# Performance work log

Measured on AMD Instinct MI355X. Metric: run time of the kernel, lower is better.

The kernel has to match this reference:

```python
import jax, jax.numpy as jnp
import numpy as np

COST_CLASS = 1.0
COST_REG = 1.0
NUM_TGT = 5  # targets per batch element, implied by `sizes = [5] * ...`

# All 5^5 = 3125 ways for each of the 5 targets to pick one of its 5 cheapest queries.
_CHOICES = np.stack(np.meshgrid(*([np.arange(NUM_TGT)] * NUM_TGT), indexing='ij'), -1).reshape(-1, NUM_TGT)


def _solve_lap5(cost):
    """Exact rectangular linear_sum_assignment for cost [num_queries, 5].

    Exchange argument: some optimal matching assigns every target (column) to one of
    its 5 cheapest queries (at most 4 of them can be taken by the other targets).
    So enumerate 5^5 candidate tuples, mask duplicates, take the argmin.
    Returns (row_ind, col_ind) sorted by row like scipy.linear_sum_assignment.
    """
    neg_vals, idx = jax.lax.top_k(-cost.T, NUM_TGT)          # [5 targets, 5 candidates]
    vals = -neg_vals
    choices = jnp.asarray(_CHOICES)                          # [3125, 5]
    t = jnp.arange(NUM_TGT)
    cand_q = idx[t[None, :], choices]                        # [3125, 5] query index per target
    cand_c = vals[t[None, :], choices]                       # [3125, 5] matching cost per target
    sq = jnp.sort(cand_q, axis=-1)
    valid = jnp.all(sq[:, 1:] != sq[:, :-1], axis=-1)        # all chosen queries distinct
    total = jnp.where(valid, cand_c.sum(-1), jnp.inf)
    best = jnp.argmin(total)
    rows = cand_q[best]                                      # [5] query index per target 0..4
    order = jnp.argsort(rows)
    return rows[order].astype(jnp.int32), order.astype(jnp.int32)


def setup_inputs() -> dict:
    key = jax.random.key(0)
    k1, k2, k3, k4 = jax.random.split(key, 4)
    bs, nq, T = 32, 2048, 32 * NUM_TGT
    return {
        'pred_logits': jax.random.normal(k1, (bs, nq, 1), dtype=jnp.float32),
        'pred_regs': jax.random.normal(k2, (bs, nq, 3), dtype=jnp.float32),
        'labels': jax.random.randint(k3, (T,), 0, 2, dtype=jnp.int32),
        'tgt_regression': jax.random.normal(k4, (T, 3), dtype=jnp.float32),
    }


def reference(pred_logits, pred_regs, labels, tgt_regression):
    bs, nq = pred_logits.shape[:2]
    # out_prob = softmax(pred_logits) is computed in the original but never used
    # (and tgt labels are unused): classification cost reduces to the constant cost_class.
    out_bbox = pred_regs.reshape(bs * nq, 3)
    # L1 cdist against ALL targets, as in the original: [bs*nq, T]
    cost_reg = jnp.sum(jnp.abs(out_bbox[:, None, :] - tgt_regression[None, :, :]), axis=-1)
    C = COST_REG * cost_reg + COST_CLASS
    # split the target axis into per-batch blocks of 5 and keep the diagonal block
    C = C.reshape(bs, nq, bs, NUM_TGT)
    b = jnp.arange(bs)
    Cb = C[b, :, b, :]                                       # [bs, nq, 5]
    rows, cols = jax.vmap(_solve_lap5)(Cb)                   # each [bs, 5]
    return rows, cols
```

## Files before the change

### kernel.cpp

```cpp
#include <hip/hip_runtime.h>

#define NUM_TGT 5

__device__ __forceinline__ bool lex_less(float c1, int q1, float c2, int q2) {
    return (c1 < c2) || (c1 == c2 && q1 < q2);
}

__device__ __forceinline__ void insert5(float c[5], int q[5], float cv, int qv) {
    if (lex_less(cv, qv, c[4], q[4])) {
        c[4] = cv; q[4] = qv;
#pragma unroll
        for (int i = 3; i >= 0; --i) {
            if (lex_less(c[i + 1], q[i + 1], c[i], q[i])) {
                float tc = c[i]; c[i] = c[i + 1]; c[i + 1] = tc;
                int   tq = q[i]; q[i] = q[i + 1]; q[i + 1] = tq;
            }
        }
    }
}

__global__ __launch_bounds__(320)
void fused_matcher_kernel(const float* __restrict__ pred_regs,
                          const float* __restrict__ tgt_reg,
                          int* __restrict__ out,
                          int bs, int nq) {
    const int b    = blockIdx.x;
    const int tid  = threadIdx.x;
    const int wave = tid >> 6;
    const int lane = tid & 63;

    __shared__ float top_c[NUM_TGT][NUM_TGT];
    __shared__ int   top_q[NUM_TGT][NUM_TGT];
    __shared__ float red_t[NUM_TGT];
    __shared__ int   red_k[NUM_TGT];

    const int bt = b * NUM_TGT + wave;
    const float t0 = tgt_reg[bt * 3 + 0];
    const float t1 = tgt_reg[bt * 3 + 1];
    const float t2 = tgt_reg[bt * 3 + 2];

    float c[5] = {INFINITY, INFINITY, INFINITY, INFINITY, INFINITY};
    int   q[5] = {0x7fffffff, 0x7fffffff, 0x7fffffff, 0x7fffffff, 0x7fffffff};

    const float* base = pred_regs + (size_t)b * nq * 3;
    for (int qi = lane; qi < nq; qi += 64) {
        float cost = fabsf(base[qi * 3 + 0] - t0);
        cost = cost + fabsf(base[qi * 3 + 1] - t1);
        cost = cost + fabsf(base[qi * 3 + 2] - t2);
        cost = cost + 1.0f;
        insert5(c, q, cost, qi);
    }

#pragma unroll
    for (int m = 1; m < 64; m <<= 1) {
#pragma unroll
        for (int i = 0; i < 5; ++i) {
            float oc = __shfl_xor(c[i], m, 64);
            int   oq = __shfl_xor(q[i], m, 64);
            insert5(c, q, oc, oq);
        }
    }

    if (lane == 0) {
#pragma unroll
        for (int i = 0; i < 5; ++i) { top_c[wave][i] = c[i]; top_q[wave][i] = q[i]; }
    }
    __syncthreads();

    float bcost = INFINITY;
    int   bk    = 0x7fffffff;
    for (int k = tid; k < 3125; k += 320) {
        int r  = k;
        const int d0 = r / 625; r -= d0 * 625;
        const int d1 = r / 125; r -= d1 * 125;
        const int d2 = r / 25;  r -= d2 * 25;
        const int d3 = r / 5;
        const int d4 = r - d3 * 5;

        const int q0 = top_q[0][d0], q1 = top_q[1][d1], q2 = top_q[2][d2],
                  q3 = top_q[3][d3], q4 = top_q[4][d4];
        const bool valid =
            q0 != q1 && q0 != q2 && q0 != q3 && q0 != q4 &&
            q1 != q2 && q1 != q3 && q1 != q4 &&
            q2 != q3 && q2 != q4 &&
            q3 != q4;

        float tot = top_c[0][d0];
        tot = tot + top_c[1][d1];
        tot = tot + top_c[2][d2];
        tot = tot + top_c[3][d3];
        tot = tot + top_c[4][d4];
        if (!valid) tot = INFINITY;

        if (tot < bcost || (tot == bcost && k < bk)) { bcost = tot; bk = k; }
    }

#pragma unroll
    for (int off = 32; off; off >>= 1) {
        float ot = __shfl_down(bcost, off, 64);
        int   ok = __shfl_down(bk, off, 64);
        if (ot < bcost || (ot == bcost && ok < bk)) { bcost = ot; bk = ok; }
    }
    if (lane == 0) { red_t[wave] = bcost; red_k[wave] = bk; }
    __syncthreads();

    if (tid == 0) {
        float fbt = red_t[0]; int fbk = red_k[0];
#pragma unroll
        for (int w = 1; w < NUM_TGT; ++w) {
            if (red_t[w] < fbt || (red_t[w] == fbt && red_k[w] < fbk)) {
                fbt = red_t[w]; fbk = red_k[w];
            }
        }
        int r = fbk;
        int d[5];
        d[0] = r / 625; r -= d[0] * 625;
        d[1] = r / 125; r -= d[1] * 125;
        d[2] = r / 25;  r -= d[2] * 25;
        d[3] = r / 5;
        d[4] = r - d[3] * 5;

        int rows[5];
#pragma unroll
        for (int t = 0; t < 5; ++t) rows[t] = top_q[t][d[t]];

#pragma unroll
        for (int i = 0; i < 5; ++i) {
            int rank = 0;
#pragma unroll
            for (int j = 0; j < 5; ++j) rank += (rows[j] < rows[i]);
            out[b * 5 + rank]          = rows[i];
            out[bs * 5 + b * 5 + rank] = i;
        }
    }
}

extern "C" void kernel_launch(void* const* d_in, const int* in_sizes, int n_in,
                              void* d_out, int out_size, void* d_ws, size_t ws_size,
                              hipStream_t stream) {
    const float* pred_regs = (const float*)d_in[1];
    const float* tgt_reg   = (const float*)d_in[3];
    int* out = (int*)d_out;

    const int T  = in_sizes[2];
    const int bs = T / NUM_TGT;
    const int nq = in_sizes[0] / bs;

    fused_matcher_kernel<<<bs, 64 * NUM_TGT, 0, stream>>>(pred_regs, tgt_reg, out, bs, nq);
}
```

Measured before the change: 83.15 us.

## Split each target's query scan across three waves with preloaded registers

The block grows from 5 to 16 waves. Fifteen of them are active, three per target, and each scans one third of the queries. Each wave loads its query values into registers up front so the loads can overlap, then keeps a local top-5. The three partial top-5 lists are merged through shared memory by five threads. The enumeration step is spread across 1024 threads. The cost is an extra barrier, a serial merge, and higher register pressure at 1024 threads per block, with only 32 blocks in total.

```diff
diff --git a/kernel.cpp b/kernel.cpp
--- a/kernel.cpp
+++ b/kernel.cpp
@@ -1,6 +1,9 @@
 #include <hip/hip_runtime.h>
 
 #define NUM_TGT 5
+#define NWAVES  16
+#define NACT    15
+#define MAXJ    11
 
 __device__ __forceinline__ bool lex_less(float c1, int q1, float c2, int q2) {
     return (c1 < c2) || (c1 == c2 && q1 < q2);
@@ -19,7 +22,7 @@
     }
 }
 
-__global__ __launch_bounds__(320)
+__global__ __launch_bounds__(1024)
 void fused_matcher_kernel(const float* __restrict__ pred_regs,
                           const float* __restrict__ tgt_reg,
                           int* __restrict__ out,
@@ -29,26 +32,61 @@
     const int wave = tid >> 6;
     const int lane = tid & 63;
 
+    __shared__ float cand_c[NACT][NUM_TGT];
+    __shared__ int   cand_q[NACT][NUM_TGT];
     __shared__ float top_c[NUM_TGT][NUM_TGT];
     __shared__ int   top_q[NUM_TGT][NUM_TGT];
-    __shared__ float red_t[NUM_TGT];
-    __shared__ int   red_k[NUM_TGT];
-
-    const int bt = b * NUM_TGT + wave;
-    const float t0 = tgt_reg[bt * 3 + 0];
-    const float t1 = tgt_reg[bt * 3 + 1];
-    const float t2 = tgt_reg[bt * 3 + 2];
+    __shared__ float red_t[NWAVES];
+    __shared__ int   red_k[NWAVES];
+
+    const bool act   = (wave < NACT);
+    const int  t     = wave / 3;
+    const int  slice = wave - t * 3;
+
+    float t0 = 0.f, t1 = 0.f, t2 = 0.f;
+    if (act) {
+        const int bt = b * NUM_TGT + t;
+        t0 = tgt_reg[bt * 3 + 0];
+        t1 = tgt_reg[bt * 3 + 1];
+        t2 = tgt_reg[bt * 3 + 2];
+    }
 
     float c[5] = {INFINITY, INFINITY, INFINITY, INFINITY, INFINITY};
     int   q[5] = {0x7fffffff, 0x7fffffff, 0x7fffffff, 0x7fffffff, 0x7fffffff};
 
     const float* base = pred_regs + (size_t)b * nq * 3;
-    for (int qi = lane; qi < nq; qi += 64) {
-        float cost = fabsf(base[qi * 3 + 0] - t0);
-        cost = cost + fabsf(base[qi * 3 + 1] - t1);
-        cost = cost + fabsf(base[qi * 3 + 2] - t2);
-        cost = cost + 1.0f;
-        insert5(c, q, cost, qi);
+
+    float v0[MAXJ], v1[MAXJ], v2[MAXJ];
+    int   qx[MAXJ];
+#pragma unroll
+    for (int j = 0; j < MAXJ; ++j) {
+        const int qi = slice * 64 + lane + j * 192;
+        const bool ok = act && (qi < nq);
+        qx[j] = ok ? qi : -1;
+        if (ok) {
+            v0[j] = base[qi * 3 + 0];
+            v1[j] = base[qi * 3 + 1];
+            v2[j] = base[qi * 3 + 2];
+        }
+    }
+#pragma unroll
+    for (int j = 0; j < MAXJ; ++j) {
+        if (qx[j] >= 0) {
+            float cost = fabsf(v0[j] - t0);
+            cost = cost + fabsf(v1[j] - t1);
+            cost = cost + fabsf(v2[j] - t2);
+            cost = cost + 1.0f;
+            insert5(c, q, cost, qx[j]);
+        }
+    }
+    if (act) {
+        for (int qi = slice * 64 + lane + MAXJ * 192; qi < nq; qi += 192) {
+            float cost = fabsf(base[qi * 3 + 0] - t0);
+            cost = cost + fabsf(base[qi * 3 + 1] - t1);
+            cost = cost + fabsf(base[qi * 3 + 2] - t2);
+            cost = cost + 1.0f;
+            insert5(c, q, cost, qi);
+        }
     }
 
 #pragma unroll
@@ -61,15 +99,29 @@
         }
     }
 
-    if (lane == 0) {
-#pragma unroll
-        for (int i = 0; i < 5; ++i) { top_c[wave][i] = c[i]; top_q[wave][i] = q[i]; }
+    if (act && lane == 0) {
+#pragma unroll
+        for (int i = 0; i < 5; ++i) { cand_c[wave][i] = c[i]; cand_q[wave][i] = q[i]; }
+    }
+    __syncthreads();
+
+    if (tid < NUM_TGT) {
+        float mc[5]; int mq[5];
+#pragma unroll
+        for (int i = 0; i < 5; ++i) { mc[i] = cand_c[tid * 3][i]; mq[i] = cand_q[tid * 3][i]; }
+#pragma unroll
+        for (int s = 1; s < 3; ++s)
+#pragma unroll
+            for (int i = 0; i < 5; ++i)
+                insert5(mc, mq, cand_c[tid * 3 + s][i], cand_q[tid * 3 + s][i]);
+#pragma unroll
+        for (int i = 0; i < 5; ++i) { top_c[tid][i] = mc[i]; top_q[tid][i] = mq[i]; }
     }
     __syncthreads();
 
     float bcost = INFINITY;
     int   bk    = 0x7fffffff;
-    for (int k = tid; k < 3125; k += 320) {
+    for (int k = tid; k < 3125; k += 1024) {
         int r  = k;
         const int d0 = r / 625; r -= d0 * 625;
         const int d1 = r / 125; r -= d1 * 125;
@@ -107,7 +159,7 @@
     if (tid == 0) {
         float fbt = red_t[0]; int fbk = red_k[0];
 #pragma unroll
-        for (int w = 1; w < NUM_TGT; ++w) {
+        for (int w = 1; w < NWAVES; ++w) {
             if (red_t[w] < fbt || (red_t[w] == fbt && red_k[w] < fbk)) {
                 fbt = red_t[w]; fbk = red_k[w];
             }
@@ -122,7 +174,7 @@
 
         int rows[5];
 #pragma unroll
-        for (int t = 0; t < 5; ++t) rows[t] = top_q[t][d[t]];
+        for (int t2i = 0; t2i < 5; ++t2i) rows[t2i] = top_q[t2i][d[t2i]];
 
 #pragma unroll
         for (int i = 0; i < 5; ++i) {
@@ -146,5 +198,5 @@
     const int bs = T / NUM_TGT;
     const int nq = in_sizes[0] / bs;
 
-    fused_matcher_kernel<<<bs, 64 * NUM_TGT, 0, stream>>>(pred_regs, tgt_reg, out, bs, nq);
-}
+    fused_matcher_kernel<<<bs, 1024, 0, stream>>>(pred_regs, tgt_reg, out, bs, nq);
+}
```

Measured after the change: 76.28 us. -8.3%, faster.
